# Optimization experiments

Hardware: AMD Instinct MI355X
Metric: run time of the kernel (lower is better)

## Reference

```python
import jax, jax.numpy as jnp
import numpy as np

ITER_ROUTING = 3          # cfg.iter_routing default in CapsNet repo
EPS = 1e-7                # tf.keras.backend.epsilon()
NUM_CAPS_IN = 1152
IN_DIM = 8
OUT_DIM = 16


def _squash(s):
    # s: [..., vec_len]; squash along the vector dimension (axis=-2 of the
    # original [B,1,16,1] layout == last axis here)
    sq = jnp.sum(s * s, axis=-1, keepdims=True)
    return (sq / (1.0 + sq)) * s / (jnp.sqrt(sq) + EPS)


def _routing(x, W, num_outputs):
    # x: [B, K, 8]  primary capsules; W: [J, K, 8, 16] per-output-capsule weights
    # u_hat[j,b,k,u] = sum_d W[j,k,d,u] * x[b,k,d]   (matmul with transpose_a)
    u_hat = jnp.einsum('jkdu,bkd->jbku', W, x)  # [J, B, K, 16]
    K = x.shape[1]
    b_IJ = jnp.zeros((K, num_outputs), dtype=x.dtype)  # logits shared across batch
    vs = []
    for j in range(num_outputs):            # sequential per original: b_IJ carries over
        uh = u_hat[j]                        # [B, K, 16]
        v = None
        for _ in range(ITER_ROUTING):
            c = jax.nn.softmax(b_IJ, axis=1)            # [K, J]
            s = jnp.einsum('k,bku->bu', c[:, j], uh)    # weighted sum over input caps
            v = _squash(s)                               # [B, 16]
            # agreement: sum over batch and vec dims of <u_hat, v>
            agree = jnp.einsum('bku,bu->k', uh, v)       # [K]
            b_IJ = b_IJ.at[:, j].add(agree)
        vs.append(v)
    # concat along capsule axis -> [B, J, 16, 1]
    return jnp.stack(vs, axis=1)[..., None]


def setup_inputs() -> dict:
    key = jax.random.key(0)
    k1, k2 = jax.random.split(key)
    B = 512
    inputs = jax.random.normal(k1, (B, NUM_CAPS_IN, IN_DIM, 1), dtype=jnp.float32)
    # original: np.random.normal(scale=0.01), one W per output capsule j
    W = 0.01 * jax.random.normal(k2, (10, NUM_CAPS_IN, IN_DIM, OUT_DIM), dtype=jnp.float32)
    return {"inputs": inputs, "W": W, "num_outputs": 10}


def reference(inputs, W, num_outputs):
    x = inputs[..., 0]  # [B, 1152, 8]
    return _routing(x, W, num_outputs)
```

## Files before the change

kernel.cpp:

```cpp
#include <hip/hip_runtime.h>

#define NB 512
#define NK 1152
#define ND 8
#define NU 16
#define NJ 10
#define NPH 30
#define EPSQ 1e-7f

#define KT 36
#define KCN 32
#define BT 16
#define BGN 32
#define XPB 292
#define WKP 140
#define SREDP 20
#define SVP 20
#define WOFF(u) ((((u) >> 1) << 4) + (((u) >> 2) << 2) + (((u) & 1) << 3))

#define OFF_BL 0
#define OFF_S  11520
#define OFF_WT (OFF_S + NPH*NB*NU)
#define WT_FLOATS (NJ*NK*NU*ND)

__global__ __launch_bounds__(256) void caps_init(const float* __restrict__ W,
                                                 float* __restrict__ bl,
                                                 float* __restrict__ s,
                                                 float* __restrict__ WT) {
  int idx = blockIdx.x * 256 + threadIdx.x;
  if (idx < NK * NJ) bl[idx] = 0.f;
  if (idx < NPH * NB * NU) s[idx] = 0.f;
  if (idx < WT_FLOATS) {
    int d = idx & 7;
    int u = (idx >> 3) & 15;
    int k = (idx >> 7) % NK;
    int j = idx / (NK * NU * ND);
    WT[idx] = W[((size_t)(j * NK + k) * ND + d) * NU + u];
  }
}

__global__ __launch_bounds__(256, 4) void caps_part(
    const float* __restrict__ x, const float* __restrict__ WT,
    const float* __restrict__ bl, float* __restrict__ sn, int js) {
  __shared__ float smem[BT * XPB + KT * WKP + KT];
  float* sx = smem;
  float* sw = smem + BT * XPB;
  float* sc = smem + BT * XPB + KT * WKP;
  float* sred = smem;
  const int tid = threadIdx.x;
  const int kc = blockIdx.x & (KCN - 1);
  const int bgi = blockIdx.x >> 5;
  const int b0 = bgi * BT;
  const int k0 = kc * KT;

  {
    const float4* gx = (const float4*)(x + (size_t)b0 * (NK * ND) + k0 * ND);
    for (int i = tid; i < BT * 72; i += 256) {
      const int b = i / 72, q = i - b * 72;
      const float4 vx = gx[(size_t)b * (NK * ND / 4) + q];
      *(float4*)&sx[b * XPB + q * 4] = vx;
    }
  }
  {
    const float4* gw = (const float4*)(WT + ((size_t)js * NK + k0) * (NU * ND));
    for (int i = tid; i < KT * 32; i += 256) {
      const int k = i >> 5, r = i & 31;
      const int u = r >> 1, h = r & 1;
      const float4 vw = gw[i];
      *(float4*)&sw[k * WKP + WOFF(u) + h * 4] = vw;
    }
  }
  if (tid < KT) {
    const float* row = bl + (size_t)(k0 + tid) * NJ;
    float r[NJ];
#pragma unroll
    for (int jj = 0; jj < NJ; ++jj) r[jj] = row[jj];
    float mx = r[0];
#pragma unroll
    for (int jj = 1; jj < NJ; ++jj) mx = fmaxf(mx, r[jj]);
    float se = 0.f;
#pragma unroll
    for (int jj = 0; jj < NJ; ++jj) se += __expf(r[jj] - mx);
    sc[tid] = __expf(r[js] - mx) / se;
  }
  __syncthreads();

  const int w = tid >> 6;
  const int lane = tid & 63;
  const int kq = lane >> 4;
  const int bq = (lane >> 2) & 3;
  const int uq = lane & 3;
  float a[4][4];
#pragma unroll
  for (int i = 0; i < 4; ++i)
#pragma unroll
    for (int m = 0; m < 4; ++m) a[i][m] = 0.f;

#pragma unroll
  for (int it = 0; it < 3; ++it) {
    const int kli = it * 4 + kq;
    if (kli < 9) {
      const int kl = w * 9 + kli;
      const float ck = sc[kl];
      float4 xa[4], xb[4];
#pragma unroll
      for (int i = 0; i < 4; ++i) {
        const float* xr = sx + (bq * 4 + i) * XPB + kl * 8;
        xa[i] = *(const float4*)xr;
        xb[i] = *(const float4*)(xr + 4);
      }
      float4 wa[4], wb[4];
      const float* wr = sw + kl * WKP + 36 * uq;
#pragma unroll
      for (int m = 0; m < 4; ++m) {
        wa[m] = *(const float4*)(wr + 8 * m);
        wb[m] = *(const float4*)(wr + 8 * m + 4);
      }
#pragma unroll
      for (int i = 0; i < 4; ++i)
#pragma unroll
        for (int m = 0; m < 4; ++m) {
          const float dot =
              xa[i].x * wa[m].x + xa[i].y * wa[m].y + xa[i].z * wa[m].z +
              xa[i].w * wa[m].w + xb[i].x * wb[m].x + xb[i].y * wb[m].y +
              xb[i].z * wb[m].z + xb[i].w * wb[m].w;
          a[i][m] = fmaf(ck, dot, a[i][m]);
        }
    }
  }
#pragma unroll
  for (int i = 0; i < 4; ++i)
#pragma unroll
    for (int m = 0; m < 4; ++m) {
      a[i][m] += __shfl_xor(a[i][m], 16, 64);
      a[i][m] += __shfl_xor(a[i][m], 32, 64);
    }
  __syncthreads();
  if (kq == 0) {
#pragma unroll
    for (int i = 0; i < 4; ++i) {
      const float4 t4 = {a[i][0], a[i][1], a[i][2], a[i][3]};
      *(float4*)&sred[(w * BT + bq * 4 + i) * SREDP + uq * 4] = t4;
    }
  }
  __syncthreads();
  {
    const int b = tid >> 4, u = tid & 15;
    const float sv =
        sred[(0 * BT + b) * SREDP + u] + sred[(1 * BT + b) * SREDP + u] +
        sred[(2 * BT + b) * SREDP + u] + sred[(3 * BT + b) * SREDP + u];
    atomicAdd(&sn[(size_t)(b0 + b) * NU + u], sv);
  }
}

__global__ __launch_bounds__(256, 4) void caps_agp(
    const float* __restrict__ x, const float* __restrict__ WT,
    const float* __restrict__ sprev, float* __restrict__ bl,
    float* __restrict__ out, int ja, int wout) {
  __shared__ float smem2[BT * XPB + KT * WKP + BT * SVP];
  float* sx = smem2;
  float* sw = smem2 + BT * XPB;
  float* sv = smem2 + BT * XPB + KT * WKP;
  const int tid = threadIdx.x;
  const int kc = blockIdx.x & (KCN - 1);
  const int bgi = blockIdx.x >> 5;
  const int b0 = bgi * BT;
  const int k0 = kc * KT;

  {
    const float4* gx = (const float4*)(x + (size_t)b0 * (NK * ND) + k0 * ND);
    for (int i = tid; i < BT * 72; i += 256) {
      const int b = i / 72, q = i - b * 72;
      const float4 vx = gx[(size_t)b * (NK * ND / 4) + q];
      *(float4*)&sx[b * XPB + q * 4] = vx;
    }
  }
  {
    const float4* gw = (const float4*)(WT + ((size_t)ja * NK + k0) * (NU * ND));
    for (int i = tid; i < KT * 32; i += 256) {
      const int k = i >> 5, r = i & 31;
      const int u = r >> 1, h = r & 1;
      const float4 vw = gw[i];
      *(float4*)&sw[k * WKP + WOFF(u) + h * 4] = vw;
    }
  }
  {
    const int b = tid >> 4, u = tid & 15;
    const float s = sprev[(size_t)(b0 + b) * NU + u];
    float sq = s * s;
    sq += __shfl_xor(sq, 1, 64);
    sq += __shfl_xor(sq, 2, 64);
    sq += __shfl_xor(sq, 4, 64);
    sq += __shfl_xor(sq, 8, 64);
    const float scale = (sq / (1.f + sq)) / (sqrtf(sq) + EPSQ);
    const float vv = scale * s;
    sv[b * SVP + u] = vv;
    if (wout && kc == 0) out[((size_t)(b0 + b) * NJ + ja) * NU + u] = vv;
  }
  __syncthreads();

  const int w = tid >> 6;
  const int lane = tid & 63;
  const int kq = lane >> 4;
  const int bq = (lane >> 2) & 3;
  const int uq = lane & 3;
  float4 vf[4];
#pragma unroll
  for (int i = 0; i < 4; ++i)
    vf[i] = *(const float4*)&sv[(bq * 4 + i) * SVP + uq * 4];

#pragma unroll
  for (int it = 0; it < 3; ++it) {
    const int kli = it * 4 + kq;
    if (kli < 9) {
      const int kl = w * 9 + kli;
      float4 xa[4], xb[4];
#pragma unroll
      for (int i = 0; i < 4; ++i) {
        const float* xr = sx + (bq * 4 + i) * XPB + kl * 8;
        xa[i] = *(const float4*)xr;
        xb[i] = *(const float4*)(xr + 4);
      }
      float4 wa[4], wb[4];
      const float* wr = sw + kl * WKP + 36 * uq;
#pragma unroll
      for (int m = 0; m < 4; ++m) {
        wa[m] = *(const float4*)(wr + 8 * m);
        wb[m] = *(const float4*)(wr + 8 * m + 4);
      }
      float ag = 0.f;
#pragma unroll
      for (int i = 0; i < 4; ++i) {
        const float4 v4 = vf[i];
        float d0 = xa[i].x * wa[0].x + xa[i].y * wa[0].y + xa[i].z * wa[0].z +
                   xa[i].w * wa[0].w + xb[i].x * wb[0].x + xb[i].y * wb[0].y +
                   xb[i].z * wb[0].z + xb[i].w * wb[0].w;
        float d1 = xa[i].x * wa[1].x + xa[i].y * wa[1].y + xa[i].z * wa[1].z +
                   xa[i].w * wa[1].w + xb[i].x * wb[1].x + xb[i].y * wb[1].y +
                   xb[i].z * wb[1].z + xb[i].w * wb[1].w;
        float d2 = xa[i].x * wa[2].x + xa[i].y * wa[2].y + xa[i].z * wa[2].z +
                   xa[i].w * wa[2].w + xb[i].x * wb[2].x + xb[i].y * wb[2].y +
                   xb[i].z * wb[2].z + xb[i].w * wb[2].w;
        float d3 = xa[i].x * wa[3].x + xa[i].y * wa[3].y + xa[i].z * wa[3].z +
                   xa[i].w * wa[3].w + xb[i].x * wb[3].x + xb[i].y * wb[3].y +
                   xb[i].z * wb[3].z + xb[i].w * wb[3].w;
        ag = fmaf(v4.x, d0, ag);
        ag = fmaf(v4.y, d1, ag);
        ag = fmaf(v4.z, d2, ag);
        ag = fmaf(v4.w, d3, ag);
      }
      ag += __shfl_xor(ag, 1, 64);
      ag += __shfl_xor(ag, 2, 64);
      ag += __shfl_xor(ag, 4, 64);
      ag += __shfl_xor(ag, 8, 64);
      if ((lane & 15) == 0)
        atomicAdd(&bl[(size_t)(k0 + kl) * NJ + ja], ag);
    }
  }
}

__global__ __launch_bounds__(256) void caps_finout(const float* __restrict__ slast,
                                                   float* __restrict__ out) {
  const int g = blockIdx.x * 256 + threadIdx.x;
  const int b = g >> 4, u = g & 15;
  const float s = slast[(size_t)b * NU + u];
  float sq = s * s;
  sq += __shfl_xor(sq, 1, 64);
  sq += __shfl_xor(sq, 2, 64);
  sq += __shfl_xor(sq, 4, 64);
  sq += __shfl_xor(sq, 8, 64);
  const float scale = (sq / (1.f + sq)) / (sqrtf(sq) + EPSQ);
  out[((size_t)b * NJ + (NJ - 1)) * NU + u] = scale * s;
}

extern "C" void kernel_launch(void* const* d_in, const int* in_sizes, int n_in,
                              void* d_out, int out_size, void* d_ws,
                              size_t ws_size, hipStream_t stream) {
  (void)in_sizes; (void)n_in; (void)out_size; (void)ws_size;
  const float* x = (const float*)d_in[0];
  const float* W = (const float*)d_in[1];
  float* out = (float*)d_out;
  float* ws = (float*)d_ws;
  float* bl = ws + OFF_BL;
  float* s  = ws + OFF_S;
  float* WT = ws + OFF_WT;

  caps_init<<<(WT_FLOATS + 255) / 256, 256, 0, stream>>>(W, bl, s, WT);
  for (int n = 0; n < NPH; ++n) {
    const int j = n / 3, t = n - 3 * j;
    if (n > 0) {
      const int ja = (t == 0) ? (j - 1) : j;
      caps_agp<<<KCN * BGN, 256, 0, stream>>>(x, WT, s + (size_t)(n - 1) * NB * NU,
                                              bl, out, ja, (t == 0) ? 1 : 0);
    }
    caps_part<<<KCN * BGN, 256, 0, stream>>>(x, WT, bl,
                                             s + (size_t)n * NB * NU, j);
  }
  caps_finout<<<(NB * NU) / 256, 256, 0, stream>>>(s + (size_t)(NPH - 1) * NB * NU,
                                                   out);
}
```

Measured before the change: 526.2 us.

## Store x and W as bf16 to halve routing-pass memory traffic

The init kernel converts the input capsules and the transposed weights to packed bf16 with round-to-nearest-even. The per-phase partial-sum and agreement kernels then load bf16 data into smaller shared-memory tiles and unpack it to fp32 for the dot products. This halves global and LDS traffic across the 59 routing launches and raises potential occupancy. In exchange, inputs and weights lose precision, which could push results past tolerance, and the unpacking adds ALU work.

```diff
diff --git a/kernel.cpp b/kernel.cpp
--- a/kernel.cpp
+++ b/kernel.cpp
@@ -1,4 +1,7 @@
 #include <hip/hip_runtime.h>
+
+typedef unsigned int uint;
+typedef unsigned short ushort_t;
 
 #define NB 512
 #define NK 1152
@@ -12,41 +15,71 @@
 #define KCN 32
 #define BT 16
 #define BGN 32
-#define XPB 292
-#define WKP 140
+#define XPH 296
+#define WPH 136
 #define SREDP 20
 #define SVP 20
-#define WOFF(u) ((((u) >> 1) << 4) + (((u) >> 2) << 2) + (((u) & 1) << 3))
 
 #define OFF_BL 0
 #define OFF_S  11520
-#define OFF_WT (OFF_S + NPH*NB*NU)
-#define WT_FLOATS (NJ*NK*NU*ND)
-
-__global__ __launch_bounds__(256) void caps_init(const float* __restrict__ W,
+#define OFF_XB 257280
+#define OFF_WTB (OFF_XB + (NB*NK*ND)/2)
+
+__device__ __forceinline__ ushort_t b16(float f) {
+  uint u = __float_as_uint(f);
+  return (ushort_t)((u + 0x7fffu + ((u >> 16) & 1u)) >> 16);
+}
+__device__ __forceinline__ void up8(const uint4 v, float* f) {
+  f[0] = __uint_as_float(v.x << 16); f[1] = __uint_as_float(v.x & 0xffff0000u);
+  f[2] = __uint_as_float(v.y << 16); f[3] = __uint_as_float(v.y & 0xffff0000u);
+  f[4] = __uint_as_float(v.z << 16); f[5] = __uint_as_float(v.z & 0xffff0000u);
+  f[6] = __uint_as_float(v.w << 16); f[7] = __uint_as_float(v.w & 0xffff0000u);
+}
+__device__ __forceinline__ float dot8(const float* a, const float* b) {
+  return a[0]*b[0] + a[1]*b[1] + a[2]*b[2] + a[3]*b[3] +
+         a[4]*b[4] + a[5]*b[5] + a[6]*b[6] + a[7]*b[7];
+}
+
+__global__ __launch_bounds__(256) void caps_init(const float* __restrict__ x,
+                                                 const float* __restrict__ W,
                                                  float* __restrict__ bl,
                                                  float* __restrict__ s,
-                                                 float* __restrict__ WT) {
-  int idx = blockIdx.x * 256 + threadIdx.x;
-  if (idx < NK * NJ) bl[idx] = 0.f;
-  if (idx < NPH * NB * NU) s[idx] = 0.f;
-  if (idx < WT_FLOATS) {
-    int d = idx & 7;
-    int u = (idx >> 3) & 15;
-    int k = (idx >> 7) % NK;
-    int j = idx / (NK * NU * ND);
-    WT[idx] = W[((size_t)(j * NK + k) * ND + d) * NU + u];
+                                                 ushort_t* __restrict__ Xb,
+                                                 ushort_t* __restrict__ WTb) {
+  const int g = blockIdx.x * 256 + threadIdx.x;
+  if (g < NK * NJ) bl[g] = 0.f;
+  if (g < NPH * NB * NU) s[g] = 0.f;
+  if (g < (NB * NK * ND) / 8) {
+    const float4* xp = (const float4*)x + (size_t)g * 2;
+    const float4 a = xp[0], b = xp[1];
+    uint4 o;
+    o.x = (uint)b16(a.x) | ((uint)b16(a.y) << 16);
+    o.y = (uint)b16(a.z) | ((uint)b16(a.w) << 16);
+    o.z = (uint)b16(b.x) | ((uint)b16(b.y) << 16);
+    o.w = (uint)b16(b.z) | ((uint)b16(b.w) << 16);
+    ((uint4*)Xb)[g] = o;
+  }
+  if (g < (NJ * NK * NU * ND) / 8) {
+    const int u = g & 15;
+    const int k = (g >> 4) % NK;
+    const int j = g / (NK * NU);
+    const float* wp = W + ((size_t)(j * NK + k) * ND) * NU + u;
+    uint4 o;
+    o.x = (uint)b16(wp[0])  | ((uint)b16(wp[16]) << 16);
+    o.y = (uint)b16(wp[32]) | ((uint)b16(wp[48]) << 16);
+    o.z = (uint)b16(wp[64]) | ((uint)b16(wp[80]) << 16);
+    o.w = (uint)b16(wp[96]) | ((uint)b16(wp[112]) << 16);
+    ((uint4*)WTb)[g] = o;
   }
 }
 
 __global__ __launch_bounds__(256, 4) void caps_part(
-    const float* __restrict__ x, const float* __restrict__ WT,
+    const ushort_t* __restrict__ Xb, const ushort_t* __restrict__ WTb,
     const float* __restrict__ bl, float* __restrict__ sn, int js) {
-  __shared__ float smem[BT * XPB + KT * WKP + KT];
-  float* sx = smem;
-  float* sw = smem + BT * XPB;
-  float* sc = smem + BT * XPB + KT * WKP;
-  float* sred = smem;
+  __shared__ __align__(16) ushort_t sxu[BT * XPH];
+  __shared__ __align__(16) ushort_t swu[KT * WPH];
+  __shared__ float sc[KT];
+  float* sred = (float*)sxu;
   const int tid = threadIdx.x;
   const int kc = blockIdx.x & (KCN - 1);
   const int bgi = blockIdx.x >> 5;
@@ -54,20 +87,19 @@
   const int k0 = kc * KT;
 
   {
-    const float4* gx = (const float4*)(x + (size_t)b0 * (NK * ND) + k0 * ND);
-    for (int i = tid; i < BT * 72; i += 256) {
-      const int b = i / 72, q = i - b * 72;
-      const float4 vx = gx[(size_t)b * (NK * ND / 4) + q];
-      *(float4*)&sx[b * XPB + q * 4] = vx;
-    }
-  }
-  {
-    const float4* gw = (const float4*)(WT + ((size_t)js * NK + k0) * (NU * ND));
-    for (int i = tid; i < KT * 32; i += 256) {
-      const int k = i >> 5, r = i & 31;
-      const int u = r >> 1, h = r & 1;
-      const float4 vw = gw[i];
-      *(float4*)&sw[k * WKP + WOFF(u) + h * 4] = vw;
+    const uint4* gx = (const uint4*)Xb + ((size_t)b0 * NK + k0);
+    for (int i = tid; i < BT * KT; i += 256) {
+      const int b = i / KT, q = i - b * KT;
+      const uint4 v = gx[(size_t)b * NK + q];
+      *(uint4*)&sxu[b * XPH + q * 8] = v;
+    }
+  }
+  {
+    const uint4* gw = (const uint4*)WTb + ((size_t)js * NK + k0) * NU;
+    for (int i = tid; i < KT * NU; i += 256) {
+      const int k = i >> 4, u = i & 15;
+      const uint4 v = gw[i];
+      *(uint4*)&swu[k * WPH + u * 8] = v;
     }
   }
   if (tid < KT) {
@@ -102,30 +134,21 @@
     if (kli < 9) {
       const int kl = w * 9 + kli;
       const float ck = sc[kl];
-      float4 xa[4], xb[4];
+      float xd[4][8];
 #pragma unroll
       for (int i = 0; i < 4; ++i) {
-        const float* xr = sx + (bq * 4 + i) * XPB + kl * 8;
-        xa[i] = *(const float4*)xr;
-        xb[i] = *(const float4*)(xr + 4);
+        const uint4 xv = *(const uint4*)&sxu[(bq * 4 + i) * XPH + kl * 8];
+        up8(xv, xd[i]);
       }
-      float4 wa[4], wb[4];
-      const float* wr = sw + kl * WKP + 36 * uq;
 #pragma unroll
       for (int m = 0; m < 4; ++m) {
-        wa[m] = *(const float4*)(wr + 8 * m);
-        wb[m] = *(const float4*)(wr + 8 * m + 4);
+        const uint4 wv = *(const uint4*)&swu[kl * WPH + (uq * 4 + m) * 8];
+        float wd[8];
+        up8(wv, wd);
+#pragma unroll
+        for (int i = 0; i < 4; ++i)
+          a[i][m] = fmaf(ck, dot8(xd[i], wd), a[i][m]);
       }
-#pragma unroll
-      for (int i = 0; i < 4; ++i)
-#pragma unroll
-        for (int m = 0; m < 4; ++m) {
-          const float dot =
-              xa[i].x * wa[m].x + xa[i].y * wa[m].y + xa[i].z * wa[m].z +
-              xa[i].w * wa[m].w + xb[i].x * wb[m].x + xb[i].y * wb[m].y +
-              xb[i].z * wb[m].z + xb[i].w * wb[m].w;
-          a[i][m] = fmaf(ck, dot, a[i][m]);
-        }
     }
   }
 #pragma unroll
@@ -154,13 +177,12 @@
 }
 
 __global__ __launch_bounds__(256, 4) void caps_agp(
-    const float* __restrict__ x, const float* __restrict__ WT,
+    const ushort_t* __restrict__ Xb, const ushort_t* __restrict__ WTb,
     const float* __restrict__ sprev, float* __restrict__ bl,
     float* __restrict__ out, int ja, int wout) {
-  __shared__ float smem2[BT * XPB + KT * WKP + BT * SVP];
-  float* sx = smem2;
-  float* sw = smem2 + BT * XPB;
-  float* sv = smem2 + BT * XPB + KT * WKP;
+  __shared__ __align__(16) ushort_t sxu[BT * XPH];
+  __shared__ __align__(16) ushort_t swu[KT * WPH];
+  __shared__ float sv[BT * SVP];
   const int tid = threadIdx.x;
   const int kc = blockIdx.x & (KCN - 1);
   const int bgi = blockIdx.x >> 5;
@@ -168,20 +190,19 @@
   const int k0 = kc * KT;
 
   {
-    const float4* gx = (const float4*)(x + (size_t)b0 * (NK * ND) + k0 * ND);
-    for (int i = tid; i < BT * 72; i += 256) {
-      const int b = i / 72, q = i - b * 72;
-      const float4 vx = gx[(size_t)b * (NK * ND / 4) + q];
-      *(float4*)&sx[b * XPB + q * 4] = vx;
-    }
-  }
-  {
-    const float4* gw = (const float4*)(WT + ((size_t)ja * NK + k0) * (NU * ND));
-    for (int i = tid; i < KT * 32; i += 256) {
-      const int k = i >> 5, r = i & 31;
-      const int u = r >> 1, h = r & 1;
-      const float4 vw = gw[i];
-      *(float4*)&sw[k * WKP + WOFF(u) + h * 4] = vw;
+    const uint4* gx = (const uint4*)Xb + ((size_t)b0 * NK + k0);
+    for (int i = tid; i < BT * KT; i += 256) {
+      const int b = i / KT, q = i - b * KT;
+      const uint4 v = gx[(size_t)b * NK + q];
+      *(uint4*)&sxu[b * XPH + q * 8] = v;
+    }
+  }
+  {
+    const uint4* gw = (const uint4*)WTb + ((size_t)ja * NK + k0) * NU;
+    for (int i = tid; i < KT * NU; i += 256) {
+      const int k = i >> 4, u = i & 15;
+      const uint4 v = gw[i];
+      *(uint4*)&swu[k * WPH + u * 8] = v;
     }
   }
   {
@@ -214,40 +235,25 @@
     const int kli = it * 4 + kq;
     if (kli < 9) {
       const int kl = w * 9 + kli;
-      float4 xa[4], xb[4];
+      float xd[4][8];
 #pragma unroll
       for (int i = 0; i < 4; ++i) {
-        const float* xr = sx + (bq * 4 + i) * XPB + kl * 8;
-        xa[i] = *(const float4*)xr;
-        xb[i] = *(const float4*)(xr + 4);
-      }
-      float4 wa[4], wb[4];
-      const float* wr = sw + kl * WKP + 36 * uq;
-#pragma unroll
-      for (int m = 0; m < 4; ++m) {
-        wa[m] = *(const float4*)(wr + 8 * m);
-        wb[m] = *(const float4*)(wr + 8 * m + 4);
+        const uint4 xv = *(const uint4*)&sxu[(bq * 4 + i) * XPH + kl * 8];
+        up8(xv, xd[i]);
       }
       float ag = 0.f;
 #pragma unroll
-      for (int i = 0; i < 4; ++i) {
-        const float4 v4 = vf[i];
-        float d0 = xa[i].x * wa[0].x + xa[i].y * wa[0].y + xa[i].z * wa[0].z +
-                   xa[i].w * wa[0].w + xb[i].x * wb[0].x + xb[i].y * wb[0].y +
-                   xb[i].z * wb[0].z + xb[i].w * wb[0].w;
-        float d1 = xa[i].x * wa[1].x + xa[i].y * wa[1].y + xa[i].z * wa[1].z +
-                   xa[i].w * wa[1].w + xb[i].x * wb[1].x + xb[i].y * wb[1].y +
-                   xb[i].z * wb[1].z + xb[i].w * wb[1].w;
-        float d2 = xa[i].x * wa[2].x + xa[i].y * wa[2].y + xa[i].z * wa[2].z +
-                   xa[i].w * wa[2].w + xb[i].x * wb[2].x + xb[i].y * wb[2].y +
-                   xb[i].z * wb[2].z + xb[i].w * wb[2].w;
-        float d3 = xa[i].x * wa[3].x + xa[i].y * wa[3].y + xa[i].z * wa[3].z +
-                   xa[i].w * wa[3].w + xb[i].x * wb[3].x + xb[i].y * wb[3].y +
-                   xb[i].z * wb[3].z + xb[i].w * wb[3].w;
-        ag = fmaf(v4.x, d0, ag);
-        ag = fmaf(v4.y, d1, ag);
-        ag = fmaf(v4.z, d2, ag);
-        ag = fmaf(v4.w, d3, ag);
+      for (int m = 0; m < 4; ++m) {
+        const uint4 wv = *(const uint4*)&swu[kl * WPH + (uq * 4 + m) * 8];
+        float wd[8];
+        up8(wv, wd);
+#pragma unroll
+        for (int i = 0; i < 4; ++i) {
+          const float vm = (m == 0) ? vf[i].x
+                         : (m == 1) ? vf[i].y
+                         : (m == 2) ? vf[i].z : vf[i].w;
+          ag = fmaf(vm, dot8(xd[i], wd), ag);
+        }
       }
       ag += __shfl_xor(ag, 1, 64);
       ag += __shfl_xor(ag, 2, 64);
@@ -283,19 +289,21 @@
   float* ws = (float*)d_ws;
   float* bl = ws + OFF_BL;
   float* s  = ws + OFF_S;
-  float* WT = ws + OFF_WT;
-
-  caps_init<<<(WT_FLOATS + 255) / 256, 256, 0, stream>>>(W, bl, s, WT);
+  ushort_t* Xb  = (ushort_t*)(ws + OFF_XB);
+  ushort_t* WTb = (ushort_t*)(ws + OFF_WTB);
+
+  caps_init<<<(NB * NK * ND / 8 + 255) / 256, 256, 0, stream>>>(x, W, bl, s,
+                                                                Xb, WTb);
   for (int n = 0; n < NPH; ++n) {
     const int j = n / 3, t = n - 3 * j;
     if (n > 0) {
       const int ja = (t == 0) ? (j - 1) : j;
-      caps_agp<<<KCN * BGN, 256, 0, stream>>>(x, WT, s + (size_t)(n - 1) * NB * NU,
-                                              bl, out, ja, (t == 0) ? 1 : 0);
-    }
-    caps_part<<<KCN * BGN, 256, 0, stream>>>(x, WT, bl,
+      caps_agp<<<KCN * BGN, 256, 0, stream>>>(
+          Xb, WTb, s + (size_t)(n - 1) * NB * NU, bl, out, ja, (t == 0) ? 1 : 0);
+    }
+    caps_part<<<KCN * BGN, 256, 0, stream>>>(Xb, WTb, bl,
                                              s + (size_t)n * NB * NU, j);
   }
-  caps_finout<<<(NB * NU) / 256, 256, 0, stream>>>(s + (size_t)(NPH - 1) * NB * NU,
-                                                   out);
-}
+  caps_finout<<<(NB * NU) / 256, 256, 0, stream>>>(
+      s + (size_t)(NPH - 1) * NB * NU, out);
+}
```

After: 490.6 us. 1.07x faster.
